# Optimization experiments

Measured on AMD Instinct MI355X. Metric: run time of the kernel, lower is better.

The kernel has to match this reference:

```python
import jax, jax.numpy as jnp
import numpy as np

B, N, F, C = 8, 4096, 1024, 64


def setup_inputs() -> dict:
    key = jax.random.key(0)
    k1, k2, k3 = jax.random.split(key, 3)
    x1 = jax.random.normal(k1, (B, N, F), dtype=jnp.float32)
    x2 = jax.random.normal(k2, (B, N, F), dtype=jnp.float32)
    W = jax.random.normal(k3, (C, F), dtype=jnp.float32) / np.sqrt(F)
    b = jnp.zeros((C,), dtype=jnp.float32)
    return {"x1": x1, "x2": x2, "W": W, "b": b}


def _select_max(x, W, b):
    # x: [B, N, F] -> scores [B, N, C]
    scores = jnp.einsum("bnf,cf->bnc", x, W) + b
    # per-batch, per-class index of max-scoring instance: [B, C]
    idx = jnp.argmax(scores, axis=1)
    # gather the selected instance feature vectors: [B, C, F]
    return jnp.take_along_axis(x, idx[:, :, None], axis=1)


def reference(x1, x2, W, b):
    d = _select_max(x1, W, b)
    d1 = _select_max(x2, W, b)
    return (d, d1)
```

## Files before the change

kernel.cpp:

```cpp
#include <hip/hip_runtime.h>

#define B_   8
#define N_   4096
#define F_   1024
#define C_   64
#define ROWS 64
#define KC   32
#define NT   (F_ / KC)
#define NBLK (N_ / ROWS)
#define MARGIN 0.08f

typedef __attribute__((ext_vector_type(8))) short bhalf8;
typedef __attribute__((ext_vector_type(4))) float f32x4;
typedef __attribute__((ext_vector_type(4))) unsigned short us4;

__device__ __forceinline__ unsigned short f2bf_rne(float x) {
    unsigned u = __builtin_bit_cast(unsigned, x);
    u += 0x7fffu + ((u >> 16) & 1u);
    return (unsigned short)(u >> 16);
}
__device__ __forceinline__ bhalf8 cvt8(float4 a, float4 b) {
    bhalf8 r;
    r[0] = (short)f2bf_rne(a.x); r[1] = (short)f2bf_rne(a.y);
    r[2] = (short)f2bf_rne(a.z); r[3] = (short)f2bf_rne(a.w);
    r[4] = (short)f2bf_rne(b.x); r[5] = (short)f2bf_rne(b.y);
    r[6] = (short)f2bf_rne(b.z); r[7] = (short)f2bf_rne(b.w);
    return r;
}
__device__ __forceinline__ void load_lds16(const void* g, void* l) {
    __builtin_amdgcn_global_load_lds(
        (const __attribute__((address_space(1))) unsigned int*)g,
        (__attribute__((address_space(3))) unsigned int*)l, 16, 0, 0);
}

#define LEXGT(a, ai, b, bi) ((a) > (b) || ((a) == (b) && (ai) < (bi)))
#define INSERT3(vv, nn)                                                        \
    do {                                                                       \
        float _v = (vv); int _n = (nn);                                        \
        if (LEXGT(_v, _n, v0, i0)) { v2=v1; i2=i1; v1=v0; i1=i0; v0=_v; i0=_n; } \
        else if (LEXGT(_v, _n, v1, i1)) { v2=v1; i2=i1; v1=_v; i1=_n; }        \
        else if (LEXGT(_v, _n, v2, i2)) { v2=_v; i2=_n; }                      \
    } while (0)

__global__ __launch_bounds__(256) void wconv_kernel(
    const float* __restrict__ W, unsigned short* __restrict__ Wh)
{
    int i = blockIdx.x * 256 + threadIdx.x;
    float4 v = ((const float4*)W)[i];
    us4 hh;
    hh[0] = f2bf_rne(v.x); hh[1] = f2bf_rne(v.y);
    hh[2] = f2bf_rne(v.z); hh[3] = f2bf_rne(v.w);
    ((us4*)Wh)[i] = hh;
}

__global__ __launch_bounds__(256, 4) void score_top_kernel(
    const float* __restrict__ x1, const float* __restrict__ x2,
    const unsigned short* __restrict__ Wh,
    float* __restrict__ pv, int* __restrict__ pi)
{
    __shared__ __align__(16) char lds[36864];

    const int tid  = threadIdx.x;
    const int nb   = blockIdx.x;
    const int b    = blockIdx.y;
    const int inp  = blockIdx.z;
    const float* __restrict__ x = inp ? x2 : x1;
    const float* __restrict__ xbase = x + ((size_t)b * N_ + (size_t)nb * ROWS) * F_;

    const int lane = tid & 63;
    const int w    = tid >> 6;
    const int rsel = lane & 15;
    const int g    = lane >> 4;

#define XOFF(buf) ((buf) * 8192)
#define WOFF(buf) (24576 + (buf) * 4096)

#define STAGE(t, buf)                                                          \
    do {                                                                       \
        const int f0_ = (t) * KC;                                              \
        _Pragma("unroll")                                                      \
        for (int j = 0; j < 2; ++j) {                                          \
            int ii = w * 2 + j;                                                \
            int r  = ii * 8 + (lane >> 3);                                     \
            int cg = (lane & 7) ^ (r & 7);                                     \
            load_lds16(xbase + (size_t)r * F_ + f0_ + cg * 4,                  \
                       lds + XOFF(buf) + ii * 1024);                           \
        }                                                                      \
        {                                                                      \
            int cls = w * 16 + (lane >> 2);                                    \
            int cg  = (lane & 3) ^ ((cls >> 1) & 3);                           \
            load_lds16(Wh + (size_t)cls * F_ + f0_ + cg * 8,                   \
                       lds + WOFF(buf) + w * 1024);                            \
        }                                                                      \
        __builtin_amdgcn_sched_barrier(0);                                     \
    } while (0)

#define COMPUTE(buf)                                                           \
    do {                                                                       \
        const char* xb = lds + XOFF(buf);                                      \
        const char* wb = lds + WOFF(buf);                                      \
        float4 xlo = *(const float4*)(xb + r_ * 128 + aswz0);                  \
        float4 xhi = *(const float4*)(xb + r_ * 128 + aswz1);                  \
        bhalf8 ah = cvt8(xlo, xhi);                                            \
        _Pragma("unroll")                                                      \
        for (int nt = 0; nt < 4; ++nt) {                                       \
            int cls = nt * 16 + rsel;                                          \
            bhalf8 bf = *(const bhalf8*)(wb + cls * 64 + ((g ^ ((cls >> 1) & 3)) * 16)); \
            acc[nt] = __builtin_amdgcn_mfma_f32_16x16x32_bf16(ah, bf, acc[nt], 0, 0, 0); \
        }                                                                      \
    } while (0)

    f32x4 acc[4];
    #pragma unroll
    for (int nt = 0; nt < 4; ++nt) acc[nt] = (f32x4){0.f, 0.f, 0.f, 0.f};

    const int r_    = w * 16 + rsel;
    const int aswz0 = ((2 * g)     ^ (r_ & 7)) * 16;
    const int aswz1 = ((2 * g + 1) ^ (r_ & 7)) * 16;

    STAGE(0, 0);
    STAGE(1, 1);

    for (int t = 0; t < NT - 2; ++t) {
        STAGE(t + 2, (t + 2) % 3);
        asm volatile("s_waitcnt vmcnt(6)" ::: "memory");
        __builtin_amdgcn_s_barrier();
        __builtin_amdgcn_sched_barrier(0);
        COMPUTE(t % 3);
        __builtin_amdgcn_sched_barrier(0);
        __builtin_amdgcn_s_barrier();
    }
    asm volatile("s_waitcnt vmcnt(3)" ::: "memory");
    __builtin_amdgcn_s_barrier();
    __builtin_amdgcn_sched_barrier(0);
    COMPUTE((NT - 2) % 3);
    asm volatile("s_waitcnt vmcnt(0)" ::: "memory");
    __builtin_amdgcn_s_barrier();
    __builtin_amdgcn_sched_barrier(0);
    COMPUTE((NT - 1) % 3);

    float wv0[4], wv1[4], wv2[4]; int wi0[4], wi1[4], wi2[4];
    #pragma unroll
    for (int nt = 0; nt < 4; ++nt) {
        float v0 = -3.4e38f, v1 = -3.4e38f, v2 = -3.4e38f;
        int   i0 = 0x7fffffff, i1 = 0x7fffffff, i2 = 0x7fffffff;
        #pragma unroll
        for (int r = 0; r < 4; ++r) {
            int n = nb * ROWS + w * 16 + 4 * g + r;
            INSERT3(acc[nt][r], n);
        }
        #pragma unroll
        for (int d = 16; d <= 32; d <<= 1) {
            float u0 = __shfl_xor(v0, d), u1 = __shfl_xor(v1, d), u2 = __shfl_xor(v2, d);
            int   j0 = __shfl_xor(i0, d), j1 = __shfl_xor(i1, d), j2 = __shfl_xor(i2, d);
            INSERT3(u0, j0); INSERT3(u1, j1); INSERT3(u2, j2);
        }
        wv0[nt] = v0; wv1[nt] = v1; wv2[nt] = v2;
        wi0[nt] = i0; wi1[nt] = i1; wi2[nt] = i2;
    }

    __syncthreads();
    float* tv = (float*)lds;
    int*   ti = (int*)(lds + 8192);
    if (lane < 16) {
        #pragma unroll
        for (int nt = 0; nt < 4; ++nt) {
            int c = nt * 16 + lane;
            tv[(w * C_ + c) * 3 + 0] = wv0[nt]; ti[(w * C_ + c) * 3 + 0] = wi0[nt];
            tv[(w * C_ + c) * 3 + 1] = wv1[nt]; ti[(w * C_ + c) * 3 + 1] = wi1[nt];
            tv[(w * C_ + c) * 3 + 2] = wv2[nt]; ti[(w * C_ + c) * 3 + 2] = wi2[nt];
        }
    }
    __syncthreads();

    if (tid < C_) {
        int c = tid;
        float v0 = -3.4e38f, v1 = -3.4e38f, v2 = -3.4e38f;
        int   i0 = 0x7fffffff, i1 = 0x7fffffff, i2 = 0x7fffffff;
        #pragma unroll
        for (int ww = 0; ww < 4; ++ww)
            #pragma unroll
            for (int k = 0; k < 3; ++k)
                INSERT3(tv[(ww * C_ + c) * 3 + k], ti[(ww * C_ + c) * 3 + k]);
        int blk = ((inp * B_ + b) * NBLK + nb);
        pv[(blk * C_ + c) * 3 + 0] = v0; pi[(blk * C_ + c) * 3 + 0] = i0;
        pv[(blk * C_ + c) * 3 + 1] = v1; pi[(blk * C_ + c) * 3 + 1] = i1;
        pv[(blk * C_ + c) * 3 + 2] = v2; pi[(blk * C_ + c) * 3 + 2] = i2;
    }
}

__global__ __launch_bounds__(256) void select_gather_kernel(
    const float* __restrict__ x1, const float* __restrict__ x2,
    const float* __restrict__ W,
    const float* __restrict__ pv, const int* __restrict__ pi,
    float* __restrict__ out)
{
    const int c   = blockIdx.x;
    const int b   = blockIdx.y;
    const int inp = blockIdx.z;
    const int tid = threadIdx.x;

    __shared__ int   s_cnt;
    __shared__ float s_m[4];
    __shared__ int   s_cand[16];
    __shared__ float s_val[16];
    __shared__ float s_wsum[4];
    __shared__ int   s_win;

    if (tid == 0) s_cnt = 0;
    __syncthreads();

    float v = -3.4e38f; int id = 0;
    if (tid < NBLK * 3) {
        int nbk = tid / 3, k = tid - nbk * 3;
        int blk = ((inp * B_ + b) * NBLK + nbk);
        int off = (blk * C_ + c) * 3 + k;
        v = pv[off]; id = pi[off];
    }
    {
        float m = v;
        #pragma unroll
        for (int d = 32; d; d >>= 1) m = fmaxf(m, __shfl_xor(m, d));
        if ((tid & 63) == 0) s_m[tid >> 6] = m;
    }
    __syncthreads();
    const float m = fmaxf(fmaxf(s_m[0], s_m[1]), fmaxf(s_m[2], s_m[3]));
    if (v >= m - MARGIN) {
        int p = atomicAdd(&s_cnt, 1);
        if (p < 16) s_cand[p] = id;
    }
    __syncthreads();

    const float* __restrict__ x = inp ? x2 : x1;
    const int ncand = min(s_cnt, 16);
    int winner;
    if (ncand == 1) {
        winner = s_cand[0];
    } else {
        for (int k = 0; k < ncand; ++k) {
            int n = s_cand[k];
            float4 xv = *(const float4*)(x + ((size_t)b * N_ + n) * F_ + tid * 4);
            float4 wq = *(const float4*)(W + (size_t)c * F_ + tid * 4);
            float p = xv.x * wq.x + xv.y * wq.y + xv.z * wq.z + xv.w * wq.w;
            #pragma unroll
            for (int d = 32; d; d >>= 1) p += __shfl_down(p, d);
            if ((tid & 63) == 0) s_wsum[tid >> 6] = p;
            __syncthreads();
            if (tid == 0) s_val[k] = s_wsum[0] + s_wsum[1] + s_wsum[2] + s_wsum[3];
            __syncthreads();
        }
        if (tid == 0) {
            float bv = s_val[0]; int bn = s_cand[0];
            for (int k = 1; k < ncand; ++k)
                if (s_val[k] > bv || (s_val[k] == bv && s_cand[k] < bn)) { bv = s_val[k]; bn = s_cand[k]; }
            s_win = bn;
        }
        __syncthreads();
        winner = s_win;
    }

    float4 vv = *(const float4*)(x + ((size_t)b * N_ + winner) * F_ + tid * 4);
    *(float4*)(out + (((size_t)inp * B_ + b) * C_ + c) * F_ + tid * 4) = vv;
}

extern "C" void kernel_launch(void* const* d_in, const int* in_sizes, int n_in,
                              void* d_out, int out_size, void* d_ws, size_t ws_size,
                              hipStream_t stream) {
    const float* x1 = (const float*)d_in[0];
    const float* x2 = (const float*)d_in[1];
    const float* W  = (const float*)d_in[2];

    unsigned short* Wh = (unsigned short*)d_ws;
    float* pv = (float*)((char*)d_ws + (size_t)C_ * F_ * sizeof(unsigned short));
    int*   pi = (int*)((char*)pv + (size_t)2 * B_ * NBLK * C_ * 3 * sizeof(float));

    wconv_kernel<<<C_ * F_ / 1024, 256, 0, stream>>>(W, Wh);
    dim3 g1(NBLK, B_, 2);
    score_top_kernel<<<g1, 256, 0, stream>>>(x1, x2, Wh, pv, pi);
    dim3 g2(C_, B_, 2);
    select_gather_kernel<<<g2, 256, 0, stream>>>(x1, x2, W, pv, pi, (float*)d_out);
}
```

Baseline: 66.11 us.

## Quad-buffer score pipeline with one barrier per step; single-wave select kernel

The score kernel moves from three to four LDS stage buffers. This lets each pipeline iteration drop one of its two workgroup barriers, since the buffer being refilled can no longer alias the one being computed. The select/gather kernel is rewritten to run as a single 64-lane wavefront. It collects candidates with ballot and shuffle instead of shared-memory atomics and barriers, and it caps the candidate count at 8 instead of 16. The larger LDS footprint (48KB per block) may lower the number of blocks resident per CU.

```diff
diff --git a/kernel.cpp b/kernel.cpp
--- a/kernel.cpp
+++ b/kernel.cpp
@@ -58,7 +58,7 @@
     const unsigned short* __restrict__ Wh,
     float* __restrict__ pv, int* __restrict__ pi)
 {
-    __shared__ __align__(16) char lds[36864];
+    __shared__ __align__(16) char lds[49152];
 
     const int tid  = threadIdx.x;
     const int nb   = blockIdx.x;
@@ -73,7 +73,7 @@
     const int g    = lane >> 4;
 
 #define XOFF(buf) ((buf) * 8192)
-#define WOFF(buf) (24576 + (buf) * 4096)
+#define WOFF(buf) (32768 + (buf) * 4096)
 
 #define STAGE(t, buf)                                                          \
     do {                                                                       \
@@ -122,22 +122,22 @@
     STAGE(1, 1);
 
     for (int t = 0; t < NT - 2; ++t) {
-        STAGE(t + 2, (t + 2) % 3);
+        STAGE(t + 2, (t + 2) & 3);
         asm volatile("s_waitcnt vmcnt(6)" ::: "memory");
-        __builtin_amdgcn_s_barrier();
-        __builtin_amdgcn_sched_barrier(0);
-        COMPUTE(t % 3);
         __builtin_amdgcn_sched_barrier(0);
         __builtin_amdgcn_s_barrier();
+        COMPUTE(t & 3);
+        __builtin_amdgcn_sched_barrier(0);
     }
     asm volatile("s_waitcnt vmcnt(3)" ::: "memory");
+    __builtin_amdgcn_sched_barrier(0);
     __builtin_amdgcn_s_barrier();
+    COMPUTE((NT - 2) & 3);
     __builtin_amdgcn_sched_barrier(0);
-    COMPUTE((NT - 2) % 3);
     asm volatile("s_waitcnt vmcnt(0)" ::: "memory");
+    __builtin_amdgcn_sched_barrier(0);
     __builtin_amdgcn_s_barrier();
-    __builtin_amdgcn_sched_barrier(0);
-    COMPUTE((NT - 1) % 3);
+    COMPUTE((NT - 1) & 3);
 
     float wv0[4], wv1[4], wv2[4]; int wi0[4], wi1[4], wi2[4];
     #pragma unroll
@@ -189,78 +189,67 @@
     }
 }
 
-__global__ __launch_bounds__(256) void select_gather_kernel(
+__global__ __launch_bounds__(64) void select_gather_kernel(
     const float* __restrict__ x1, const float* __restrict__ x2,
     const float* __restrict__ W,
     const float* __restrict__ pv, const int* __restrict__ pi,
     float* __restrict__ out)
 {
-    const int c   = blockIdx.x;
-    const int b   = blockIdx.y;
-    const int inp = blockIdx.z;
-    const int tid = threadIdx.x;
-
-    __shared__ int   s_cnt;
-    __shared__ float s_m[4];
-    __shared__ int   s_cand[16];
-    __shared__ float s_val[16];
-    __shared__ float s_wsum[4];
-    __shared__ int   s_win;
-
-    if (tid == 0) s_cnt = 0;
-    __syncthreads();
-
-    float v = -3.4e38f; int id = 0;
-    if (tid < NBLK * 3) {
-        int nbk = tid / 3, k = tid - nbk * 3;
-        int blk = ((inp * B_ + b) * NBLK + nbk);
-        int off = (blk * C_ + c) * 3 + k;
-        v = pv[off]; id = pi[off];
-    }
-    {
-        float m = v;
-        #pragma unroll
-        for (int d = 32; d; d >>= 1) m = fmaxf(m, __shfl_xor(m, d));
-        if ((tid & 63) == 0) s_m[tid >> 6] = m;
-    }
-    __syncthreads();
-    const float m = fmaxf(fmaxf(s_m[0], s_m[1]), fmaxf(s_m[2], s_m[3]));
-    if (v >= m - MARGIN) {
-        int p = atomicAdd(&s_cnt, 1);
-        if (p < 16) s_cand[p] = id;
-    }
-    __syncthreads();
+    const int c    = blockIdx.x;
+    const int b    = blockIdx.y;
+    const int inp  = blockIdx.z;
+    const int lane = threadIdx.x;
+
+    const int blk  = ((inp * B_ + b) * NBLK + lane);
+    const int base = (blk * C_ + c) * 3;
+    const float v0 = pv[base + 0], v1 = pv[base + 1], v2 = pv[base + 2];
+    const int   j0 = pi[base + 0], j1 = pi[base + 1], j2 = pi[base + 2];
+
+    float m = v0;
+    #pragma unroll
+    for (int d = 32; d; d >>= 1) m = fmaxf(m, __shfl_xor(m, d));
+    const float thr = m - MARGIN;
+
+    int cand[8]; int nc = 0;
+    #pragma unroll
+    for (int k = 0; k < 3; ++k) {
+        float vk = k == 0 ? v0 : (k == 1 ? v1 : v2);
+        int   jk = k == 0 ? j0 : (k == 1 ? j1 : j2);
+        unsigned long long mask = __ballot(vk >= thr);
+        while (mask) {
+            int l = __ffsll(mask) - 1; mask &= mask - 1;
+            int n = __shfl(jk, l);
+            if (nc < 8) cand[nc++] = n;
+        }
+    }
 
     const float* __restrict__ x = inp ? x2 : x1;
-    const int ncand = min(s_cnt, 16);
     int winner;
-    if (ncand == 1) {
-        winner = s_cand[0];
+    if (nc == 1) {
+        winner = cand[0];
     } else {
-        for (int k = 0; k < ncand; ++k) {
-            int n = s_cand[k];
-            float4 xv = *(const float4*)(x + ((size_t)b * N_ + n) * F_ + tid * 4);
-            float4 wq = *(const float4*)(W + (size_t)c * F_ + tid * 4);
-            float p = xv.x * wq.x + xv.y * wq.y + xv.z * wq.z + xv.w * wq.w;
+        float bv = -3.4e38f; int bn = 0x7fffffff;
+        const float4* wrow = (const float4*)(W + (size_t)c * F_) + lane * 4;
+        for (int k = 0; k < nc; ++k) {
+            int n = cand[k];
+            const float4* xrow = (const float4*)(x + ((size_t)b * N_ + n) * F_) + lane * 4;
+            float p = 0.f;
             #pragma unroll
-            for (int d = 32; d; d >>= 1) p += __shfl_down(p, d);
-            if ((tid & 63) == 0) s_wsum[tid >> 6] = p;
-            __syncthreads();
-            if (tid == 0) s_val[k] = s_wsum[0] + s_wsum[1] + s_wsum[2] + s_wsum[3];
-            __syncthreads();
-        }
-        if (tid == 0) {
-            float bv = s_val[0]; int bn = s_cand[0];
-            for (int k = 1; k < ncand; ++k)
-                if (s_val[k] > bv || (s_val[k] == bv && s_cand[k] < bn)) { bv = s_val[k]; bn = s_cand[k]; }
-            s_win = bn;
-        }
-        __syncthreads();
-        winner = s_win;
-    }
-
-    float4 vv = *(const float4*)(x + ((size_t)b * N_ + winner) * F_ + tid * 4);
-    *(float4*)(out + (((size_t)inp * B_ + b) * C_ + c) * F_ + tid * 4) = vv;
+            for (int q = 0; q < 4; ++q) {
+                float4 xv = xrow[q], wq = wrow[q];
+                p += xv.x * wq.x + xv.y * wq.y + xv.z * wq.z + xv.w * wq.w;
+            }
+            #pragma unroll
+            for (int d = 32; d; d >>= 1) p += __shfl_xor(p, d);
+            if (p > bv || (p == bv && n < bn)) { bv = p; bn = n; }
+        }
+        winner = bn;
+    }
+
+    const float4* src = (const float4*)(x + ((size_t)b * N_ + winner) * F_);
+    float4* dst = (float4*)(out + (((size_t)inp * B_ + b) * C_ + c) * F_);
+    #pragma unroll
+    for (int q = 0; q < 4; ++q) dst[lane + 64 * q] = src[lane + 64 * q];
 }
 
 extern "C" void kernel_launch(void* const* d_in, const int* in_sizes, int n_in,
@@ -278,5 +267,5 @@
     dim3 g1(NBLK, B_, 2);
     score_top_kernel<<<g1, 256, 0, stream>>>(x1, x2, Wh, pv, pi);
     dim3 g2(C_, B_, 2);
-    select_gather_kernel<<<g2, 256, 0, stream>>>(x1, x2, W, pv, pi, (float*)d_out);
-}
+    select_gather_kernel<<<g2, 64, 0, stream>>>(x1, x2, W, pv, pi, (float*)d_out);
+}
```

Measured after the change: 85.13 us. 28.8% more time.

## Halve rows per block, switch to double-buffered pipeline, keep top-2 candidates

Applied to the files above, without the earlier changes.

The score kernel now takes 32 rows per block with 128 threads, which doubles the grid, and shrinks LDS from 36KB to 16KB so more blocks fit per CU. The triple-buffered, vmcnt-tuned pipeline becomes a simple double buffer with one __syncthreads per K step. Each block keeps only its top-2 candidates, so select_gather reads exactly 256 entries with one per thread. In exchange each block reloads W twice as often, the simpler pipeline hides less load latency, and top-2 per block reduces the margin-candidate safety.

```diff
diff --git a/kernel.cpp b/kernel.cpp
--- a/kernel.cpp
+++ b/kernel.cpp
@@ -4,7 +4,7 @@
 #define N_   4096
 #define F_   1024
 #define C_   64
-#define ROWS 64
+#define ROWS 32
 #define KC   32
 #define NT   (F_ / KC)
 #define NBLK (N_ / ROWS)
@@ -34,6 +34,12 @@
 }
 
 #define LEXGT(a, ai, b, bi) ((a) > (b) || ((a) == (b) && (ai) < (bi)))
+#define INSERT2(vv, nn)                                                        \
+    do {                                                                       \
+        float _v = (vv); int _n = (nn);                                        \
+        if (LEXGT(_v, _n, v0, i0)) { v1=v0; i1=i0; v0=_v; i0=_n; }             \
+        else if (LEXGT(_v, _n, v1, i1)) { v1=_v; i1=_n; }                      \
+    } while (0)
 #define INSERT3(vv, nn)                                                        \
     do {                                                                       \
         float _v = (vv); int _n = (nn);                                        \
@@ -53,12 +59,12 @@
     ((us4*)Wh)[i] = hh;
 }
 
-__global__ __launch_bounds__(256, 4) void score_top_kernel(
+__global__ __launch_bounds__(128, 4) void score_top_kernel(
     const float* __restrict__ x1, const float* __restrict__ x2,
     const unsigned short* __restrict__ Wh,
     float* __restrict__ pv, int* __restrict__ pi)
 {
-    __shared__ __align__(16) char lds[36864];
+    __shared__ __align__(16) char lds[16384];
 
     const int tid  = threadIdx.x;
     const int nb   = blockIdx.x;
@@ -72,27 +78,28 @@
     const int rsel = lane & 15;
     const int g    = lane >> 4;
 
-#define XOFF(buf) ((buf) * 8192)
-#define WOFF(buf) (24576 + (buf) * 4096)
+#define XOFF(buf) ((buf) * 4096)
+#define WOFF(buf) (8192 + (buf) * 4096)
 
 #define STAGE(t, buf)                                                          \
     do {                                                                       \
         const int f0_ = (t) * KC;                                              \
         _Pragma("unroll")                                                      \
         for (int j = 0; j < 2; ++j) {                                          \
-            int ii = w * 2 + j;                                                \
+            int ii = w * 2 + j;                        \
             int r  = ii * 8 + (lane >> 3);                                     \
             int cg = (lane & 7) ^ (r & 7);                                     \
             load_lds16(xbase + (size_t)r * F_ + f0_ + cg * 4,                  \
                        lds + XOFF(buf) + ii * 1024);                           \
         }                                                                      \
-        {                                                                      \
-            int cls = w * 16 + (lane >> 2);                                    \
+        _Pragma("unroll")                                                      \
+        for (int j = 0; j < 2; ++j) {                                          \
+            int wi  = w * 2 + j;                      \
+            int cls = wi * 16 + (lane >> 2);                                   \
             int cg  = (lane & 3) ^ ((cls >> 1) & 3);                           \
             load_lds16(Wh + (size_t)cls * F_ + f0_ + cg * 8,                   \
-                       lds + WOFF(buf) + w * 1024);                            \
+                       lds + WOFF(buf) + wi * 1024);                           \
         }                                                                      \
-        __builtin_amdgcn_sched_barrier(0);                                     \
     } while (0)
 
 #define COMPUTE(buf)                                                           \
@@ -119,25 +126,14 @@
     const int aswz1 = ((2 * g + 1) ^ (r_ & 7)) * 16;
 
     STAGE(0, 0);
-    STAGE(1, 1);
-
-    for (int t = 0; t < NT - 2; ++t) {
-        STAGE(t + 2, (t + 2) % 3);
-        asm volatile("s_waitcnt vmcnt(6)" ::: "memory");
-        __builtin_amdgcn_s_barrier();
-        __builtin_amdgcn_sched_barrier(0);
-        COMPUTE(t % 3);
-        __builtin_amdgcn_sched_barrier(0);
-        __builtin_amdgcn_s_barrier();
-    }
-    asm volatile("s_waitcnt vmcnt(3)" ::: "memory");
-    __builtin_amdgcn_s_barrier();
-    __builtin_amdgcn_sched_barrier(0);
-    COMPUTE((NT - 2) % 3);
-    asm volatile("s_waitcnt vmcnt(0)" ::: "memory");
-    __builtin_amdgcn_s_barrier();
-    __builtin_amdgcn_sched_barrier(0);
-    COMPUTE((NT - 1) % 3);
+    __syncthreads();
+
+    for (int t = 0; t < NT; ++t) {
+        const int cur = t & 1;
+        if (t + 1 < NT) STAGE(t + 1, cur ^ 1);
+        COMPUTE(cur);
+        __syncthreads();
+    }
 
     float wv0[4], wv1[4], wv2[4]; int wi0[4], wi1[4], wi2[4];
     #pragma unroll
@@ -161,7 +157,7 @@
 
     __syncthreads();
     float* tv = (float*)lds;
-    int*   ti = (int*)(lds + 8192);
+    int*   ti = (int*)(lds + 4096);
     if (lane < 16) {
         #pragma unroll
         for (int nt = 0; nt < 4; ++nt) {
@@ -175,17 +171,16 @@
 
     if (tid < C_) {
         int c = tid;
-        float v0 = -3.4e38f, v1 = -3.4e38f, v2 = -3.4e38f;
-        int   i0 = 0x7fffffff, i1 = 0x7fffffff, i2 = 0x7fffffff;
-        #pragma unroll
-        for (int ww = 0; ww < 4; ++ww)
+        float v0 = -3.4e38f, v1 = -3.4e38f;
+        int   i0 = 0x7fffffff, i1 = 0x7fffffff;
+        #pragma unroll
+        for (int ww = 0; ww < 2; ++ww)
             #pragma unroll
             for (int k = 0; k < 3; ++k)
-                INSERT3(tv[(ww * C_ + c) * 3 + k], ti[(ww * C_ + c) * 3 + k]);
+                INSERT2(tv[(ww * C_ + c) * 3 + k], ti[(ww * C_ + c) * 3 + k]);
         int blk = ((inp * B_ + b) * NBLK + nb);
-        pv[(blk * C_ + c) * 3 + 0] = v0; pi[(blk * C_ + c) * 3 + 0] = i0;
-        pv[(blk * C_ + c) * 3 + 1] = v1; pi[(blk * C_ + c) * 3 + 1] = i1;
-        pv[(blk * C_ + c) * 3 + 2] = v2; pi[(blk * C_ + c) * 3 + 2] = i2;
+        pv[(blk * C_ + c) * 2 + 0] = v0; pi[(blk * C_ + c) * 2 + 0] = i0;
+        pv[(blk * C_ + c) * 2 + 1] = v1; pi[(blk * C_ + c) * 2 + 1] = i1;
     }
 }
 
@@ -210,13 +205,11 @@
     if (tid == 0) s_cnt = 0;
     __syncthreads();
 
-    float v = -3.4e38f; int id = 0;
-    if (tid < NBLK * 3) {
-        int nbk = tid / 3, k = tid - nbk * 3;
-        int blk = ((inp * B_ + b) * NBLK + nbk);
-        int off = (blk * C_ + c) * 3 + k;
-        v = pv[off]; id = pi[off];
-    }
+    const int nbk = tid >> 1, k = tid & 1;
+    const int blk = ((inp * B_ + b) * NBLK + nbk);
+    const int off = (blk * C_ + c) * 2 + k;
+    const float v = pv[off];
+    const int  id = pi[off];
     {
         float m = v;
         #pragma unroll
@@ -237,8 +230,8 @@
     if (ncand == 1) {
         winner = s_cand[0];
     } else {
-        for (int k = 0; k < ncand; ++k) {
-            int n = s_cand[k];
+        for (int k2 = 0; k2 < ncand; ++k2) {
+            int n = s_cand[k2];
             float4 xv = *(const float4*)(x + ((size_t)b * N_ + n) * F_ + tid * 4);
             float4 wq = *(const float4*)(W + (size_t)c * F_ + tid * 4);
             float p = xv.x * wq.x + xv.y * wq.y + xv.z * wq.z + xv.w * wq.w;
@@ -246,13 +239,13 @@
             for (int d = 32; d; d >>= 1) p += __shfl_down(p, d);
             if ((tid & 63) == 0) s_wsum[tid >> 6] = p;
             __syncthreads();
-            if (tid == 0) s_val[k] = s_wsum[0] + s_wsum[1] + s_wsum[2] + s_wsum[3];
+            if (tid == 0) s_val[k2] = s_wsum[0] + s_wsum[1] + s_wsum[2] + s_wsum[3];
             __syncthreads();
         }
         if (tid == 0) {
             float bv = s_val[0]; int bn = s_cand[0];
-            for (int k = 1; k < ncand; ++k)
-                if (s_val[k] > bv || (s_val[k] == bv && s_cand[k] < bn)) { bv = s_val[k]; bn = s_cand[k]; }
+            for (int k2 = 1; k2 < ncand; ++k2)
+                if (s_val[k2] > bv || (s_val[k2] == bv && s_cand[k2] < bn)) { bv = s_val[k2]; bn = s_cand[k2]; }
             s_win = bn;
         }
         __syncthreads();
@@ -272,11 +265,11 @@
 
     unsigned short* Wh = (unsigned short*)d_ws;
     float* pv = (float*)((char*)d_ws + (size_t)C_ * F_ * sizeof(unsigned short));
-    int*   pi = (int*)((char*)pv + (size_t)2 * B_ * NBLK * C_ * 3 * sizeof(float));
+    int*   pi = (int*)((char*)pv + (size_t)2 * B_ * NBLK * C_ * 2 * sizeof(float));
 
     wconv_kernel<<<C_ * F_ / 1024, 256, 0, stream>>>(W, Wh);
     dim3 g1(NBLK, B_, 2);
-    score_top_kernel<<<g1, 256, 0, stream>>>(x1, x2, Wh, pv, pi);
+    score_top_kernel<<<g1, 128, 0, stream>>>(x1, x2, Wh, pv, pi);
     dim3 g2(C_, B_, 2);
     select_gather_kernel<<<g2, 256, 0, stream>>>(x1, x2, W, pv, pi, (float*)d_out);
 }
```

Result: no change. 66.58 us (+0.7%).
